# Kernel optimization log

Hardware: AMD Instinct MI355X
Metric: run time of the kernel (lower is better)

The kernel has to match this reference:

```python
import jax, jax.numpy as jnp
import numpy as np

HIDDEN = 768
HEADS = 12
HEAD_DIM = HIDDEN // HEADS

def setup_inputs() -> dict:
    key = jax.random.key(0)
    ks = jax.random.split(key, 9)
    B, S = 1, 4096
    s = 1.0 / np.sqrt(HIDDEN)
    x = jax.random.normal(ks[0], (B, S, HIDDEN), dtype=jnp.float32)
    # per-head Q/K/V linear weights stacked: [H, D, dh]
    Wq = jax.random.uniform(ks[1], (HEADS, HIDDEN, HEAD_DIM), jnp.float32, -s, s)
    Wk = jax.random.uniform(ks[2], (HEADS, HIDDEN, HEAD_DIM), jnp.float32, -s, s)
    Wv = jax.random.uniform(ks[3], (HEADS, HIDDEN, HEAD_DIM), jnp.float32, -s, s)
    bq = jax.random.uniform(ks[4], (HEADS, HEAD_DIM), jnp.float32, -s, s)
    bk = jax.random.uniform(ks[5], (HEADS, HEAD_DIM), jnp.float32, -s, s)
    bv = jax.random.uniform(ks[6], (HEADS, HEAD_DIM), jnp.float32, -s, s)
    Wo = jax.random.uniform(ks[7], (HIDDEN, HIDDEN), jnp.float32, -s, s)
    bo = jax.random.uniform(ks[8], (HIDDEN,), jnp.float32, -s, s)
    return {"x": x, "Wq": Wq, "Wk": Wk, "Wv": Wv, "bq": bq, "bk": bk, "bv": bv, "Wo": Wo, "bo": bo}

def reference(x, Wq, Wk, Wv, bq, bk, bv, Wo, bo):
    # x: [B,S,D]; per-head projections batched over heads
    q = jnp.einsum('bsd,hde->bhse', x, Wq) + bq[None, :, None, :]  # [B,H,S,dh]
    k = jnp.einsum('bsd,hde->bhse', x, Wk) + bk[None, :, None, :]
    v = jnp.einsum('bsd,hde->bhse', x, Wv) + bv[None, :, None, :]
    scale = 1.0 / np.sqrt(HEAD_DIM)
    scores = jnp.einsum('bhse,bhte->bhst', q, k) * scale  # [B,H,S,S]
    probs = jax.nn.softmax(scores, axis=-1)
    ctx = jnp.einsum('bhst,bhte->bhse', probs, v)  # [B,H,S,dh]
    B, H, S, dh = ctx.shape
    concat = ctx.transpose(0, 2, 1, 3).reshape(B, S, H * dh)  # head concat along last dim
    return concat @ Wo + bo
```

## Files before the change

kernel.cpp:

```cpp
#include <hip/hip_runtime.h>
#include <hip/hip_bf16.h>
#include <cstdint>
#include <cstddef>

#define HIDDEN 768
#define HEADS 12
#define HD 64
#define SEQ 4096
#define NSPLIT 8

typedef __hip_bfloat16 bf16;
typedef short bf16x8 __attribute__((ext_vector_type(8)));
typedef float f32x4 __attribute__((ext_vector_type(4)));

#define QSCALE 0.18033688011112042f

static __device__ __forceinline__ void gload_lds16(const bf16* g, bf16* l) {
  __builtin_amdgcn_global_load_lds(
      (const __attribute__((address_space(1))) unsigned int*)(g),
      (__attribute__((address_space(3))) unsigned int*)(l), 16, 0, 0);
}

static __device__ __forceinline__ unsigned cvt_pk_bf16(float lo, float hi) {
  unsigned r;
  asm("v_cvt_pk_bf16_f32 %0, %1, %2" : "=v"(r) : "v"(lo), "v"(hi));
  return r;
}

static __device__ __forceinline__ float b2f(short s) {
  union { unsigned u; float f; } v;
  v.u = ((unsigned)(unsigned short)s) << 16;
  return v.f;
}

__global__ __launch_bounds__(256) void prep_kernel(
    const float* __restrict__ x, const float* __restrict__ Wq,
    const float* __restrict__ Wk, const float* __restrict__ Wv,
    const float* __restrict__ Wo, bf16* __restrict__ xb,
    bf16* __restrict__ Wt, bf16* __restrict__ Wot) {
  __shared__ float t[64][65];
  int i = blockIdx.x;
  if (i < 3072) {
    int idx = i * 256 + threadIdx.x;
    float4 v = ((const float4*)x)[idx];
    union { bf16 h[4]; short4 s4; } u;
    u.h[0] = __float2bfloat16(v.x);
    u.h[1] = __float2bfloat16(v.y);
    u.h[2] = __float2bfloat16(v.z);
    u.h[3] = __float2bfloat16(v.w);
    ((short4*)xb)[idx] = u.s4;
    return;
  }
  i -= 3072;
  const float* src;
  bf16* dst;
  int R, C, tr, tc;
  if (i < 432) {
    int m = i / 144;
    int j = i - m * 144;
    int b = j / 12;
    tr = j - b * 12; tc = 0;
    src = (m == 0 ? Wq : m == 1 ? Wk : Wv) + (size_t)b * 768 * 64;
    dst = Wt + (size_t)m * 589824 + (size_t)b * 768 * 64;
    R = 768; C = 64;
  } else {
    int j = i - 432;
    tr = j / 12; tc = j - tr * 12;
    src = Wo; dst = Wot; R = 768; C = 768;
  }
  int r0 = tr << 6, c0 = tc << 6;
#pragma unroll
  for (int k = threadIdx.x; k < 4096; k += 256) {
    int r = k >> 6, c = k & 63;
    t[r][c] = src[(size_t)(r0 + r) * C + c0 + c];
  }
  __syncthreads();
#pragma unroll
  for (int k = threadIdx.x; k < 4096; k += 256) {
    int c = k >> 6, r = k & 63;
    dst[(size_t)(c0 + c) * R + r0 + r] = __float2bfloat16(t[r][c]);
  }
}

template <int EPI>
__global__ __launch_bounds__(256) void gemm_kernel(
    const bf16* __restrict__ A, const bf16* __restrict__ Bt,
    int M, int N, int K, int ntn,
    const float* __restrict__ bq, const float* __restrict__ bk,
    const float* __restrict__ bv,
    bf16* __restrict__ Qb, bf16* __restrict__ Kb, bf16* __restrict__ Vt,
    const float* __restrict__ bo, float* __restrict__ outp) {
  __shared__ bf16 sA[2][128 * 32];
  __shared__ bf16 sB[2][128 * 32];
  __shared__ bf16 strans[4][16][20];

  int bid = blockIdx.x;
  int bm = bid / ntn, bn = bid - bm * ntn;
  int tid = threadIdx.x;
  int w = tid >> 6, l = tid & 63;
  int wr = w >> 1, wc = w & 1;
  int l15 = l & 15, g = l >> 4;

  const bf16* Ab = A + (size_t)bm * 128 * K;
  const bf16* Bb = Bt + (size_t)bn * 128 * K;

  int sr = tid >> 2;
  int sc = (tid & 3) << 3;

  f32x4 acc[4][4] = {};
  int NT = K >> 5;
  int cur = 0;

  auto stage = [&](int buf, int kt) {
    const bf16* ga = Ab + (size_t)sr * K + kt * 32 + sc;
    const bf16* gb = Bb + (size_t)sr * K + kt * 32 + sc;
    bf16* la = &sA[buf][w << 9];
    bf16* lb = &sB[buf][w << 9];
    gload_lds16(ga, la);
    gload_lds16(ga + (size_t)64 * K, la + 2048);
    gload_lds16(gb, lb);
    gload_lds16(gb + (size_t)64 * K, lb + 2048);
  };

  stage(0, 0);
  for (int kt = 0; kt < NT; ++kt) {
    __syncthreads();
    if (kt + 1 < NT) stage(cur ^ 1, kt + 1);
    const bf16* pa = &sA[cur][0];
    const bf16* pb = &sB[cur][0];
    bf16x8 af[4], bfr[4];
#pragma unroll
    for (int m = 0; m < 4; ++m)
      af[m] = *(const bf16x8*)&pa[(wr * 64 + m * 16 + l15) * 32 + g * 8];
#pragma unroll
    for (int n = 0; n < 4; ++n)
      bfr[n] = *(const bf16x8*)&pb[(wc * 64 + n * 16 + l15) * 32 + g * 8];
#pragma unroll
    for (int m = 0; m < 4; ++m)
#pragma unroll
      for (int n = 0; n < 4; ++n)
        acc[m][n] = __builtin_amdgcn_mfma_f32_16x16x32_bf16(af[m], bfr[n], acc[m][n], 0, 0, 0);
    cur ^= 1;
  }

  if (EPI == 0) {
#pragma unroll
    for (int n = 0; n < 4; ++n) {
      int j = bn * 128 + wc * 64 + n * 16 + l15;
      int mat = j / 768;
      int jj = j - mat * 768;
      int h = jj >> 6, e = jj & 63;
      const float* bias = (mat == 0) ? bq : (mat == 1) ? bk : bv;
      float bb = bias[h * 64 + e];
      float scl = (mat == 0) ? QSCALE : 1.0f;
#pragma unroll
      for (int m = 0; m < 4; ++m) {
        int s0m = bm * 128 + wr * 64 + m * 16;
        if (mat < 2) {
          bf16* dst = (mat == 0 ? Qb : Kb) + (size_t)h * SEQ * 64;
#pragma unroll
          for (int r = 0; r < 4; ++r)
            dst[(size_t)(s0m + g * 4 + r) * 64 + e] = __float2bfloat16((acc[m][n][r] + bb) * scl);
        } else {
#pragma unroll
          for (int r = 0; r < 4; ++r)
            strans[w][g * 4 + r][l15] = __float2bfloat16(acc[m][n][r] + bb);
          int e0f = e - l15;
          bf16* dst = Vt + (size_t)h * SEQ * 64;
#pragma unroll
          for (int r = 0; r < 4; ++r) {
            bf16 val = strans[w][l15][g * 4 + r];
            dst[(size_t)(e0f + g * 4 + r) * SEQ + s0m + l15] = val;
          }
        }
      }
    }
  } else {
#pragma unroll
    for (int n = 0; n < 4; ++n) {
      int j = bn * 128 + wc * 64 + n * 16 + l15;
      float bb = bo[j];
#pragma unroll
      for (int m = 0; m < 4; ++m) {
        int s0m = bm * 128 + wr * 64 + m * 16;
#pragma unroll
        for (int r = 0; r < 4; ++r)
          outp[(size_t)(s0m + g * 4 + r) * HIDDEN + j] = acc[m][n][r] + bb;
      }
    }
  }
}

__global__ __launch_bounds__(512) void flash_kernel(
    const bf16* __restrict__ Qb, const bf16* __restrict__ Kb,
    const bf16* __restrict__ Vt, bf16* __restrict__ partC,
    float* __restrict__ partM, float* __restrict__ partL) {
  __shared__ bf16 sK[2][64 * 64];
  __shared__ bf16 sV[2][64 * 64];

  const int head = blockIdx.y;
  const int split = blockIdx.z;
  const int w = threadIdx.x >> 6, l = threadIdx.x & 63;
  const int l15 = l & 15, g = l >> 4;
  const int sw = l15 & 7;
  const int q0w = blockIdx.x * 128 + w * 16;

  const bf16* Qh = Qb + (size_t)head * SEQ * 64;
  const bf16* Kh = Kb + (size_t)head * SEQ * 64;
  const bf16* Vh = Vt + (size_t)head * SEQ * 64;

  bf16x8 aq[2];
  aq[0] = *(const bf16x8*)&Qh[(size_t)(q0w + l15) * 64 + g * 8];
  aq[1] = *(const bf16x8*)&Qh[(size_t)(q0w + l15) * 64 + 32 + g * 8];

  float mrun = -1e30f, lsum = 0.f;
  f32x4 cacc[4] = {};

  const int lr8 = l >> 3;
  const int csrc = (l & 7) ^ lr8;

  auto stage = [&](int buf, int kt) {
    int t0 = kt * 64;
    const bf16* gk = Kh + (size_t)(t0 + w * 8 + lr8) * 64 + csrc * 8;
    gload_lds16(gk, &sK[buf][(w * 8) * 64]);
    const bf16* gv = Vh + (size_t)(w * 8 + lr8) * SEQ + t0 + csrc * 8;
    gload_lds16(gv, &sV[buf][(w * 8) * 64]);
  };

  const int kt0 = split * (SEQ / 64 / NSPLIT);
  const int kt1 = kt0 + SEQ / 64 / NSPLIT;
  stage(0, kt0);
  int cur = 0;
  const bool ge = (l & 16) == 0;

  for (int kt = kt0; kt < kt1; ++kt) {
    __syncthreads();
    if (kt + 1 < kt1) stage(cur ^ 1, kt + 1);
    const bf16* kb = &sK[cur][0];
    const bf16* vb = &sV[cur][0];

    f32x4 sc8[4] = {};
    __builtin_amdgcn_s_setprio(1);
#pragma unroll
    for (int n = 0; n < 4; ++n) {
      bf16x8 b0 = *(const bf16x8*)&kb[(n * 16 + l15) * 64 + (g ^ sw) * 8];
      bf16x8 b1 = *(const bf16x8*)&kb[(n * 16 + l15) * 64 + ((4 + g) ^ sw) * 8];
      sc8[n] = __builtin_amdgcn_mfma_f32_16x16x32_bf16(b0, aq[0], sc8[n], 0, 0, 0);
      sc8[n] = __builtin_amdgcn_mfma_f32_16x16x32_bf16(b1, aq[1], sc8[n], 0, 0, 0);
    }
    __builtin_amdgcn_s_setprio(0);

    float vm = fmaxf(fmaxf(fmaxf(sc8[0][0], sc8[0][1]), fmaxf(sc8[0][2], sc8[0][3])),
                     fmaxf(fmaxf(sc8[1][0], sc8[1][1]), fmaxf(sc8[1][2], sc8[1][3])));
    vm = fmaxf(vm, fmaxf(fmaxf(fmaxf(sc8[2][0], sc8[2][1]), fmaxf(sc8[2][2], sc8[2][3])),
                         fmaxf(fmaxf(sc8[3][0], sc8[3][1]), fmaxf(sc8[3][2], sc8[3][3]))));
    vm = fmaxf(vm, __shfl_xor(vm, 16));
    vm = fmaxf(vm, __shfl_xor(vm, 32));

    if (__any(vm > mrun + 8.0f)) {
      float mn = fmaxf(mrun, vm);
      float a = __builtin_amdgcn_exp2f(mrun - mn);
      mrun = mn;
      lsum *= a;
      float aqr[4];
#pragma unroll
      for (int r = 0; r < 4; ++r) aqr[r] = __shfl(a, g * 4 + r);
#pragma unroll
      for (int f = 0; f < 4; ++f)
#pragma unroll
        for (int r = 0; r < 4; ++r) cacc[f][r] *= aqr[r];
    }

    unsigned X[4][2];
    float ls0 = 0.f, ls1 = 0.f;
#pragma unroll
    for (int n = 0; n < 4; ++n) {
#pragma unroll
      for (int h = 0; h < 2; ++h) {
        float p0 = __builtin_amdgcn_exp2f(sc8[n][2 * h] - mrun);
        float p1 = __builtin_amdgcn_exp2f(sc8[n][2 * h + 1] - mrun);
        ls0 += p0; ls1 += p1;
        X[n][h] = cvt_pk_bf16(p0, p1);
      }
    }
    lsum += ls0 + ls1;

#pragma unroll
    for (int kkl = 0; kkl < 2; ++kkl) {
      unsigned P0 = X[2 * kkl][0], Q0 = X[2 * kkl + 1][0];
      unsigned P1 = X[2 * kkl][1], Q1 = X[2 * kkl + 1][1];
      asm("v_permlane32_swap_b32 %0, %1" : "+v"(P0), "+v"(Q0));
      asm("v_permlane32_swap_b32 %0, %1" : "+v"(P1), "+v"(Q1));
      unsigned sP0 = __shfl_xor((int)P0, 16);
      unsigned sQ0 = __shfl_xor((int)Q0, 16);
      unsigned sP1 = __shfl_xor((int)P1, 16);
      unsigned sQ1 = __shfl_xor((int)Q1, 16);
      union { unsigned u[4]; bf16x8 v8; } ap;
      ap.u[0] = ge ? P0 : sQ0;
      ap.u[1] = ge ? P1 : sQ1;
      ap.u[2] = ge ? sP0 : Q0;
      ap.u[3] = ge ? sP1 : Q1;
      __builtin_amdgcn_s_setprio(1);
#pragma unroll
      for (int f = 0; f < 4; ++f) {
        bf16x8 bv8 = *(const bf16x8*)&vb[(f * 16 + l15) * 64 + ((kkl * 4 + g) ^ sw) * 8];
        cacc[f] = __builtin_amdgcn_mfma_f32_16x16x32_bf16(ap.v8, bv8, cacc[f], 0, 0, 0);
      }
      __builtin_amdgcn_s_setprio(0);
    }
    cur ^= 1;
  }

  float s = lsum;
  s += __shfl_xor(s, 16);
  s += __shfl_xor(s, 32);

  bf16* pcw = partC + (size_t)split * SEQ * HIDDEN;
#pragma unroll
  for (int f = 0; f < 4; ++f)
#pragma unroll
    for (int r = 0; r < 4; ++r)
      pcw[(size_t)(q0w + g * 4 + r) * HIDDEN + head * 64 + f * 16 + l15] =
          __float2bfloat16(cacc[f][r]);
  if (l < 16) {
    size_t mi = (size_t)split * HEADS * SEQ + (size_t)head * SEQ + q0w + l15;
    partM[mi] = mrun;
    partL[mi] = s;
  }
}

__global__ __launch_bounds__(256) void combine_kernel(
    const bf16* __restrict__ partC, const float* __restrict__ partM,
    const float* __restrict__ partL, bf16* __restrict__ ctx) {
  int i = blockIdx.x * 256 + threadIdx.x;
  int idx = i * 4;
  int s = idx / HIDDEN, c = idx - s * HIDDEN;
  int h = c >> 6;
  size_t mi = (size_t)h * SEQ + s;
  float m[NSPLIT], lv[NSPLIT];
  float ms = -1e30f;
#pragma unroll
  for (int sp = 0; sp < NSPLIT; ++sp) {
    m[sp] = partM[(size_t)sp * HEADS * SEQ + mi];
    lv[sp] = partL[(size_t)sp * HEADS * SEQ + mi];
    ms = fmaxf(ms, m[sp]);
  }
  float wgt[NSPLIT];
  float denom = 0.f;
#pragma unroll
  for (int sp = 0; sp < NSPLIT; ++sp) {
    wgt[sp] = __builtin_amdgcn_exp2f(m[sp] - ms);
    denom += lv[sp] * wgt[sp];
  }
  float inv = 1.0f / denom;
  float ax = 0.f, ay = 0.f, az = 0.f, aw = 0.f;
#pragma unroll
  for (int sp = 0; sp < NSPLIT; ++sp) {
    short4 c4 = ((const short4*)(partC + (size_t)sp * SEQ * HIDDEN))[i];
    ax += b2f(c4.x) * wgt[sp];
    ay += b2f(c4.y) * wgt[sp];
    az += b2f(c4.z) * wgt[sp];
    aw += b2f(c4.w) * wgt[sp];
  }
  union { bf16 h4[4]; short4 s4; } u;
  u.h4[0] = __float2bfloat16(ax * inv);
  u.h4[1] = __float2bfloat16(ay * inv);
  u.h4[2] = __float2bfloat16(az * inv);
  u.h4[3] = __float2bfloat16(aw * inv);
  ((short4*)ctx)[i] = u.s4;
}

extern "C" void kernel_launch(void* const* d_in, const int* in_sizes, int n_in,
                              void* d_out, int out_size, void* d_ws, size_t ws_size,
                              hipStream_t stream) {
  const float* x = (const float*)d_in[0];
  const float* Wq = (const float*)d_in[1];
  const float* Wk = (const float*)d_in[2];
  const float* Wv = (const float*)d_in[3];
  const float* bq = (const float*)d_in[4];
  const float* bk = (const float*)d_in[5];
  const float* bv = (const float*)d_in[6];
  const float* Wo = (const float*)d_in[7];
  const float* bo = (const float*)d_in[8];
  float* outp = (float*)d_out;

  char* ws = (char*)d_ws;
  bf16* xb = (bf16*)ws;   ws += (size_t)SEQ * HIDDEN * 2;
  bf16* Wt = (bf16*)ws;   ws += (size_t)3 * HIDDEN * HIDDEN * 2;
  bf16* Wot = (bf16*)ws;  ws += (size_t)HIDDEN * HIDDEN * 2;
  bf16* Qb = (bf16*)ws;   ws += (size_t)SEQ * HIDDEN * 2;
  bf16* Kb = (bf16*)ws;   ws += (size_t)SEQ * HIDDEN * 2;
  bf16* Vt = (bf16*)ws;   ws += (size_t)SEQ * HIDDEN * 2;
  bf16* ctx = (bf16*)ws;  ws += (size_t)SEQ * HIDDEN * 2;
  bf16* partC = (bf16*)ws;  ws += (size_t)NSPLIT * SEQ * HIDDEN * 2;
  float* partM = (float*)ws; ws += (size_t)NSPLIT * HEADS * SEQ * 4;
  float* partL = (float*)ws; ws += (size_t)NSPLIT * HEADS * SEQ * 4;

  prep_kernel<<<3648, 256, 0, stream>>>(x, Wq, Wk, Wv, Wo, xb, Wt, Wot);

  gemm_kernel<0><<<32 * 18, 256, 0, stream>>>(xb, Wt, SEQ, 2304, 768, 18,
                                              bq, bk, bv, Qb, Kb, Vt, nullptr, nullptr);

  flash_kernel<<<dim3(SEQ / 128, HEADS, NSPLIT), 512, 0, stream>>>(Qb, Kb, Vt,
                                                                   partC, partM, partL);
  combine_kernel<<<SEQ * HIDDEN / 4 / 256, 256, 0, stream>>>(partC, partM, partL, ctx);

  gemm_kernel<1><<<32 * 6, 256, 0, stream>>>(ctx, Wot, SEQ, 768, 768, 6,
                                             nullptr, nullptr, nullptr, nullptr, nullptr,
                                             nullptr, bo, outp);
}
```

Before: 150.5 us.

## Software-pipeline flash attention: overlap previous PV with current QK, triple-buffer V

```diff
diff --git a/kernel.cpp b/kernel.cpp
--- a/kernel.cpp
+++ b/kernel.cpp
@@ -31,6 +31,10 @@
   union { unsigned u; float f; } v;
   v.u = ((unsigned)(unsigned short)s) << 16;
   return v.f;
+}
+
+static __device__ __forceinline__ float max3f(float a, float b, float c) {
+  return fmaxf(fmaxf(a, b), c);
 }
 
 __global__ __launch_bounds__(256) void prep_kernel(
@@ -196,7 +200,7 @@
     const bf16* __restrict__ Vt, bf16* __restrict__ partC,
     float* __restrict__ partM, float* __restrict__ partL) {
   __shared__ bf16 sK[2][64 * 64];
-  __shared__ bf16 sV[2][64 * 64];
+  __shared__ bf16 sV[3][64 * 64];
 
   const int head = blockIdx.y;
   const int split = blockIdx.z;
@@ -218,42 +222,35 @@
 
   const int lr8 = l >> 3;
   const int csrc = (l & 7) ^ lr8;
-
-  auto stage = [&](int buf, int kt) {
+  const bool ge = (l & 16) == 0;
+
+  auto stage = [&](int kt) {
     int t0 = kt * 64;
     const bf16* gk = Kh + (size_t)(t0 + w * 8 + lr8) * 64 + csrc * 8;
-    gload_lds16(gk, &sK[buf][(w * 8) * 64]);
+    gload_lds16(gk, &sK[kt & 1][(w * 8) * 64]);
     const bf16* gv = Vh + (size_t)(w * 8 + lr8) * SEQ + t0 + csrc * 8;
-    gload_lds16(gv, &sV[buf][(w * 8) * 64]);
+    gload_lds16(gv, &sV[kt % 3][(w * 8) * 64]);
   };
 
-  const int kt0 = split * (SEQ / 64 / NSPLIT);
-  const int kt1 = kt0 + SEQ / 64 / NSPLIT;
-  stage(0, kt0);
-  int cur = 0;
-  const bool ge = (l & 16) == 0;
-
-  for (int kt = kt0; kt < kt1; ++kt) {
-    __syncthreads();
-    if (kt + 1 < kt1) stage(cur ^ 1, kt + 1);
-    const bf16* kb = &sK[cur][0];
-    const bf16* vb = &sV[cur][0];
-
-    f32x4 sc8[4] = {};
+  auto qk = [&](const bf16* kb, f32x4 (&sc)[4]) {
     __builtin_amdgcn_s_setprio(1);
 #pragma unroll
     for (int n = 0; n < 4; ++n) {
       bf16x8 b0 = *(const bf16x8*)&kb[(n * 16 + l15) * 64 + (g ^ sw) * 8];
       bf16x8 b1 = *(const bf16x8*)&kb[(n * 16 + l15) * 64 + ((4 + g) ^ sw) * 8];
-      sc8[n] = __builtin_amdgcn_mfma_f32_16x16x32_bf16(b0, aq[0], sc8[n], 0, 0, 0);
-      sc8[n] = __builtin_amdgcn_mfma_f32_16x16x32_bf16(b1, aq[1], sc8[n], 0, 0, 0);
+      sc[n] = __builtin_amdgcn_mfma_f32_16x16x32_bf16(b0, aq[0], sc[n], 0, 0, 0);
+      sc[n] = __builtin_amdgcn_mfma_f32_16x16x32_bf16(b1, aq[1], sc[n], 0, 0, 0);
     }
     __builtin_amdgcn_s_setprio(0);
-
-    float vm = fmaxf(fmaxf(fmaxf(sc8[0][0], sc8[0][1]), fmaxf(sc8[0][2], sc8[0][3])),
-                     fmaxf(fmaxf(sc8[1][0], sc8[1][1]), fmaxf(sc8[1][2], sc8[1][3])));
-    vm = fmaxf(vm, fmaxf(fmaxf(fmaxf(sc8[2][0], sc8[2][1]), fmaxf(sc8[2][2], sc8[2][3])),
-                         fmaxf(fmaxf(sc8[3][0], sc8[3][1]), fmaxf(sc8[3][2], sc8[3][3]))));
+  };
+
+  auto softmax_step = [&](f32x4 (&sc)[4], unsigned (&X)[4][2]) {
+    float m0 = max3f(sc[0][0], sc[0][1], sc[0][2]);
+    float m1 = max3f(sc[0][3], sc[1][0], sc[1][1]);
+    float m2 = max3f(sc[1][2], sc[1][3], sc[2][0]);
+    float m3 = max3f(sc[2][1], sc[2][2], sc[2][3]);
+    float m4 = max3f(sc[3][0], sc[3][1], sc[3][2]);
+    float vm = fmaxf(max3f(m0, m1, m2), max3f(m3, m4, sc[3][3]));
     vm = fmaxf(vm, __shfl_xor(vm, 16));
     vm = fmaxf(vm, __shfl_xor(vm, 32));
 
@@ -271,20 +268,21 @@
         for (int r = 0; r < 4; ++r) cacc[f][r] *= aqr[r];
     }
 
-    unsigned X[4][2];
     float ls0 = 0.f, ls1 = 0.f;
 #pragma unroll
     for (int n = 0; n < 4; ++n) {
 #pragma unroll
       for (int h = 0; h < 2; ++h) {
-        float p0 = __builtin_amdgcn_exp2f(sc8[n][2 * h] - mrun);
-        float p1 = __builtin_amdgcn_exp2f(sc8[n][2 * h + 1] - mrun);
+        float p0 = __builtin_amdgcn_exp2f(sc[n][2 * h] - mrun);
+        float p1 = __builtin_amdgcn_exp2f(sc[n][2 * h + 1] - mrun);
         ls0 += p0; ls1 += p1;
         X[n][h] = cvt_pk_bf16(p0, p1);
       }
     }
     lsum += ls0 + ls1;
-
+  };
+
+  auto pv = [&](unsigned (&X)[4][2], const bf16* vb) {
 #pragma unroll
     for (int kkl = 0; kkl < 2; ++kkl) {
       unsigned P0 = X[2 * kkl][0], Q0 = X[2 * kkl + 1][0];
@@ -308,8 +306,31 @@
       }
       __builtin_amdgcn_s_setprio(0);
     }
-    cur ^= 1;
-  }
+  };
+
+  const int kt0 = split * (SEQ / 64 / NSPLIT);
+  const int kt1 = kt0 + SEQ / 64 / NSPLIT;
+
+  stage(kt0);
+  stage(kt0 + 1);
+  __syncthreads();
+
+  unsigned Xp[4][2];
+  {
+    f32x4 sc[4] = {};
+    qk(&sK[kt0 & 1][0], sc);
+    softmax_step(sc, Xp);
+  }
+
+  for (int t = kt0 + 1; t < kt1; ++t) {
+    __syncthreads();
+    if (t + 1 < kt1) stage(t + 1);
+    pv(Xp, &sV[(t - 1) % 3][0]);
+    f32x4 sc[4] = {};
+    qk(&sK[t & 1][0], sc);
+    softmax_step(sc, Xp);
+  }
+  pv(Xp, &sV[(kt1 - 1) % 3][0]);
 
   float s = lsum;
   s += __shfl_xor(s, 16);
```

Result: no change. 150.8 us (+0.2%).
